# Optimization experiments

Hardware: AMD Instinct MI355X
Metric: run time of the kernel (lower is better)

Reference implementation:

```python
import jax, jax.numpy as jnp
import numpy as np

DIM = 1024
HIDDEN = 2816
NUM_EXPERTS = 8
TOP_K = 2
BATCH, SEQ = 2, 2048


def setup_inputs() -> dict:
    key = jax.random.key(0)
    kx, k1, k2, k3, kg = jax.random.split(key, 5)
    x = jax.random.normal(kx, (BATCH, SEQ, DIM), dtype=jnp.float32)
    # merged expert weights, layout (num_experts * hidden, dim) as in torch module
    w1 = jax.random.normal(k1, (NUM_EXPERTS * HIDDEN, DIM), dtype=jnp.float32) * 0.02
    w2 = jax.random.normal(k2, (NUM_EXPERTS * HIDDEN, DIM), dtype=jnp.float32) * 0.02
    w3 = jax.random.normal(k3, (NUM_EXPERTS * HIDDEN, DIM), dtype=jnp.float32) * 0.02
    gate_w = jax.random.normal(kg, (NUM_EXPERTS, DIM), dtype=jnp.float32) * 0.02
    return {"x": x, "w1": w1, "w2": w2, "w3": w3, "gate_w": gate_w}


def reference(x, w1, w2, w3, gate_w):
    input_shape = x.shape
    xt = x.reshape(-1, input_shape[-1])  # (T, D)
    T = xt.shape[0]
    # gating: softmax in fp32, top-k, renormalize selected weights
    logits = xt @ gate_w.T  # (T, E)
    probs = jax.nn.softmax(logits.astype(jnp.float32), axis=-1)
    weights, selected = jax.lax.top_k(probs, TOP_K)  # (T, K)
    weights = weights / jnp.sum(weights, axis=-1, keepdims=True)
    weights = weights.astype(x.dtype)
    # combine weights per expert: (T, E)
    combine = jnp.sum(jax.nn.one_hot(selected, NUM_EXPERTS, dtype=x.dtype) * weights[..., None], axis=1)
    # per-expert SwiGLU FFN: h = silu(x W1_e^T) * (x W3_e^T); out_e = h @ W2_e
    W1 = w1.reshape(NUM_EXPERTS, HIDDEN, DIM)
    W2 = w2.reshape(NUM_EXPERTS, HIDDEN, DIM)
    W3 = w3.reshape(NUM_EXPERTS, HIDDEN, DIM)
    y = jnp.zeros((T, DIM), dtype=x.dtype)
    for e in range(NUM_EXPERTS):  # fixed small expert loop
        h = jax.nn.silu(xt @ W1[e].T) * (xt @ W3[e].T)  # (T, H)
        y = y + (h @ W2[e]) * combine[:, e:e + 1]
    return y.reshape(input_shape)
```

## Files before the change

### kernel.cpp

```cpp
#include <hip/hip_runtime.h>
#include <cstddef>
#include <cstdint>

#define T_TOK 4096
#define DIM   1024
#define HID   2816
#define NE    8
#define TOPK  2
#define CAP   9216
#define NRT   72

#define BM 128
#define BN 64
#define BK 32

#define WS_COUNTS  0
#define WS_CURSORS 64
#define WS_OFFSETS 128
#define WS_TILE_E  256
#define WS_SEL     1024
#define WS_WTS     (WS_SEL  + T_TOK*2*4)
#define WS_ATOK    (WS_WTS  + T_TOK*2*4)
#define WS_AW      (WS_ATOK + CAP*4)
#define WS_H       140288

typedef __attribute__((ext_vector_type(8))) short bf16x8;
typedef __attribute__((ext_vector_type(4))) float f32x4;

__device__ __forceinline__ unsigned short f2bf(float f) {
  unsigned int u = __builtin_bit_cast(unsigned int, f);
  unsigned int r = u + 0x7FFFu + ((u >> 16) & 1u);
  return (unsigned short)(r >> 16);
}
__device__ __forceinline__ float bf2f(unsigned short s) {
  unsigned int u = ((unsigned int)s) << 16;
  return __builtin_bit_cast(float, u);
}
__device__ __forceinline__ void split2(float f, unsigned short& hi, unsigned short& lo) {
  hi = f2bf(f);
  lo = f2bf(f - bf2f(hi));
}

__device__ __forceinline__ int fragoff(int row, int k) {
  return ((row >> 4) << 9) + ((k >> 3) << 7) + ((row & 15) << 3) + (k & 7);
}

__global__ __launch_bounds__(256) void gate_kernel(
    const float* __restrict__ x, const float* __restrict__ gw,
    int* __restrict__ sel, float* __restrict__ wts, int* __restrict__ counts)
{
  const int wave = threadIdx.x >> 6;
  const int lane = threadIdx.x & 63;
  const int t = blockIdx.x * 4 + wave;

  const float* xr = x + (size_t)t * DIM;
  float acc[NE] = {0.f, 0.f, 0.f, 0.f, 0.f, 0.f, 0.f, 0.f};

#pragma unroll 4
  for (int j = 0; j < DIM / 64; ++j) {
    const int d = lane + 64 * j;
    const float xv = xr[d];
#pragma unroll
    for (int e = 0; e < NE; ++e) acc[e] = fmaf(xv, gw[e * DIM + d], acc[e]);
  }
#pragma unroll
  for (int m = 32; m > 0; m >>= 1) {
#pragma unroll
    for (int e = 0; e < NE; ++e) acc[e] += __shfl_xor(acc[e], m, 64);
  }

  if (lane == 0) {
    float mx = acc[0];
#pragma unroll
    for (int e = 1; e < NE; ++e) mx = fmaxf(mx, acc[e]);
    float ex[NE];
#pragma unroll
    for (int e = 0; e < NE; ++e) ex[e] = __expf(acc[e] - mx);
    int e0 = 0; float p0 = ex[0];
#pragma unroll
    for (int e = 1; e < NE; ++e) if (ex[e] > p0) { p0 = ex[e]; e0 = e; }
    int e1 = -1; float p1 = -1.f;
#pragma unroll
    for (int e = 0; e < NE; ++e) if (e != e0 && ex[e] > p1) { p1 = ex[e]; e1 = e; }
    const float inv = 1.f / (p0 + p1);
    sel[2 * t + 0] = e0; sel[2 * t + 1] = e1;
    wts[2 * t + 0] = p0 * inv; wts[2 * t + 1] = p1 * inv;
    atomicAdd(&counts[e0], 1);
    atomicAdd(&counts[e1], 1);
  }
}

__global__ void offsets_kernel(const int* __restrict__ counts,
                               int* __restrict__ offsets, int* __restrict__ cursors,
                               int* __restrict__ tile_e)
{
  if (threadIdx.x == 0 && blockIdx.x == 0) {
    int off = 0;
    for (int e = 0; e < NE; ++e) {
      offsets[e] = off;
      cursors[e] = off;
      off += (counts[e] + 127) & ~127;
    }
    offsets[NE] = off;
    for (int t = 0; t < NRT; ++t) {
      const int r = t * BM;
      int ee = 0;
      while (ee < NE - 1 && r >= offsets[ee + 1]) ++ee;
      tile_e[t] = ee;
    }
  }
}

__global__ __launch_bounds__(256) void scatter_kernel(
    const int* __restrict__ sel, const float* __restrict__ wts,
    int* __restrict__ cursors, int* __restrict__ atok, float* __restrict__ aw)
{
  const int t = blockIdx.x * 256 + threadIdx.x;
  if (t < T_TOK) {
#pragma unroll
    for (int k = 0; k < TOPK; ++k) {
      const int e = sel[2 * t + k];
      const int pos = atomicAdd(&cursors[e], 1);
      atok[pos] = t;
      aw[pos] = wts[2 * t + k];
    }
  }
}

__global__ __launch_bounds__(256, 2) void gemm1_kernel(
    const float* __restrict__ x, const float* __restrict__ w1,
    const float* __restrict__ w3, const int* __restrict__ atok,
    const int* __restrict__ tile_e, float* __restrict__ h,
    int hc0, int CH)
{
  __shared__ unsigned short sAh[4096], sAl[4096];
  __shared__ unsigned short sB1h[2048], sB1l[2048];
  __shared__ unsigned short sB3h[2048], sB3l[2048];
  __shared__ int sToks[BM];

  const int rt = blockIdx.x, ct = blockIdx.y;
  const int row0 = rt * BM;
  const int tid = threadIdx.x;
  const int lane = tid & 63;
  const int wv = tid >> 6, wr = wv >> 1, wc = wv & 1;
  const int e = tile_e[rt];

  if (tid < BM) {
    const int tk = atok[row0 + tid];
    sToks[tid] = tk < 0 ? 0 : tk;
  }
  __syncthreads();

  const int c4 = tid & 7;
  const int srow = tid >> 3;
  const float* ax[4];
  int aadr[4];
#pragma unroll
  for (int i = 0; i < 4; ++i) {
    const int r = srow + 32 * i;
    ax[i] = x + (size_t)sToks[r] * DIM + c4 * 4;
    aadr[i] = fragoff(r, c4 * 4);
  }
  const float* W1p = w1 + ((size_t)e * HID + hc0 + ct * BN) * DIM;
  const float* W3p = w3 + ((size_t)e * HID + hc0 + ct * BN) * DIM;
  const float* b1p[2]; const float* b3p[2];
  int badr[2];
#pragma unroll
  for (int i = 0; i < 2; ++i) {
    const int c = srow + 32 * i;
    b1p[i] = W1p + (size_t)c * DIM + c4 * 4;
    b3p[i] = W3p + (size_t)c * DIM + c4 * 4;
    badr[i] = fragoff(c, c4 * 4);
  }

  const f32x4 vz = {0.f, 0.f, 0.f, 0.f};
  f32x4 acc1[4][2], acc3[4][2];
#pragma unroll
  for (int i = 0; i < 4; ++i)
#pragma unroll
    for (int j = 0; j < 2; ++j) { acc1[i][j] = vz; acc3[i][j] = vz; }

  for (int kt = 0; kt < DIM / BK; ++kt) {
    const int k0 = kt * BK;
    float4 av[4], b1v[2], b3v[2];
#pragma unroll
    for (int i = 0; i < 4; ++i) av[i] = *(const float4*)(ax[i] + k0);
#pragma unroll
    for (int i = 0; i < 2; ++i) {
      b1v[i] = *(const float4*)(b1p[i] + k0);
      b3v[i] = *(const float4*)(b3p[i] + k0);
    }
    __syncthreads();
#pragma unroll
    for (int i = 0; i < 4; ++i) {
      ushort4 hi, lo;
      split2(av[i].x, hi.x, lo.x); split2(av[i].y, hi.y, lo.y);
      split2(av[i].z, hi.z, lo.z); split2(av[i].w, hi.w, lo.w);
      *(ushort4*)&sAh[aadr[i]] = hi;  *(ushort4*)&sAl[aadr[i]] = lo;
    }
#pragma unroll
    for (int i = 0; i < 2; ++i) {
      ushort4 hi, lo;
      split2(b1v[i].x, hi.x, lo.x); split2(b1v[i].y, hi.y, lo.y);
      split2(b1v[i].z, hi.z, lo.z); split2(b1v[i].w, hi.w, lo.w);
      *(ushort4*)&sB1h[badr[i]] = hi; *(ushort4*)&sB1l[badr[i]] = lo;
      split2(b3v[i].x, hi.x, lo.x); split2(b3v[i].y, hi.y, lo.y);
      split2(b3v[i].z, hi.z, lo.z); split2(b3v[i].w, hi.w, lo.w);
      *(ushort4*)&sB3h[badr[i]] = hi; *(ushort4*)&sB3l[badr[i]] = lo;
    }
    __syncthreads();

    bf16x8 ah[4], al[4], g1h[2], g1l[2], g3h[2], g3l[2];
#pragma unroll
    for (int ar = 0; ar < 4; ++ar) {
      const int rb = wr * 4 + ar;
      ah[ar] = *(const bf16x8*)&sAh[rb * 512 + lane * 8];
      al[ar] = *(const bf16x8*)&sAl[rb * 512 + lane * 8];
    }
#pragma unroll
    for (int bc = 0; bc < 2; ++bc) {
      const int cb = wc * 2 + bc;
      g1h[bc] = *(const bf16x8*)&sB1h[cb * 512 + lane * 8];
      g1l[bc] = *(const bf16x8*)&sB1l[cb * 512 + lane * 8];
      g3h[bc] = *(const bf16x8*)&sB3h[cb * 512 + lane * 8];
      g3l[bc] = *(const bf16x8*)&sB3l[cb * 512 + lane * 8];
    }
#pragma unroll
    for (int ar = 0; ar < 4; ++ar)
#pragma unroll
      for (int bc = 0; bc < 2; ++bc) {
        acc1[ar][bc] = __builtin_amdgcn_mfma_f32_16x16x32_bf16(ah[ar], g1h[bc], acc1[ar][bc], 0, 0, 0);
        acc1[ar][bc] = __builtin_amdgcn_mfma_f32_16x16x32_bf16(ah[ar], g1l[bc], acc1[ar][bc], 0, 0, 0);
        acc1[ar][bc] = __builtin_amdgcn_mfma_f32_16x16x32_bf16(al[ar], g1h[bc], acc1[ar][bc], 0, 0, 0);
        acc3[ar][bc] = __builtin_amdgcn_mfma_f32_16x16x32_bf16(ah[ar], g3h[bc], acc3[ar][bc], 0, 0, 0);
        acc3[ar][bc] = __builtin_amdgcn_mfma_f32_16x16x32_bf16(ah[ar], g3l[bc], acc3[ar][bc], 0, 0, 0);
        acc3[ar][bc] = __builtin_amdgcn_mfma_f32_16x16x32_bf16(al[ar], g3h[bc], acc3[ar][bc], 0, 0, 0);
      }
  }

#pragma unroll
  for (int ar = 0; ar < 4; ++ar)
#pragma unroll
    for (int bc = 0; bc < 2; ++bc)
#pragma unroll
      for (int r = 0; r < 4; ++r) {
        const int row = row0 + wr * 64 + ar * 16 + (lane >> 4) * 4 + r;
        const int col = ct * BN + wc * 32 + bc * 16 + (lane & 15);
        const float g = acc1[ar][bc][r];
        const float u = acc3[ar][bc][r];
        const float s = g / (1.f + __expf(-g));
        h[(size_t)row * CH + col] = s * u;
      }
}

__global__ __launch_bounds__(256, 2) void gemm2_kernel(
    const float* __restrict__ h, const float* __restrict__ w2,
    const int* __restrict__ atok, const float* __restrict__ aw,
    const int* __restrict__ tile_e, float* __restrict__ y,
    int hc0, int CH)
{
  __shared__ unsigned short sAh[4096], sAl[4096];
  __shared__ unsigned short sBh[2048], sBl[2048];

  const int rt = blockIdx.x, ct = blockIdx.y;
  const int row0 = rt * BM;
  const int tid = threadIdx.x;
  const int lane = tid & 63;
  const int wv = tid >> 6, wr = wv >> 1, wc = wv & 1;
  const int e = tile_e[rt];

  const int c4 = tid & 7;
  const int srow = tid >> 3;
  const float* ax[4];
  int aadr[4];
#pragma unroll
  for (int i = 0; i < 4; ++i) {
    const int r = srow + 32 * i;
    ax[i] = h + (size_t)(row0 + r) * CH + c4 * 4;
    aadr[i] = fragoff(r, c4 * 4);
  }
  const int n = tid & 63;
  const int kq0 = tid >> 6;
  const float* W2p = w2 + ((size_t)e * HID + hc0) * DIM + (size_t)ct * BN + n;

  const f32x4 vz = {0.f, 0.f, 0.f, 0.f};
  f32x4 acc[4][2];
#pragma unroll
  for (int i = 0; i < 4; ++i)
#pragma unroll
    for (int j = 0; j < 2; ++j) acc[i][j] = vz;

  for (int kt = 0; kt < CH / BK; ++kt) {
    const int k0 = kt * BK;
    float4 av[4];
    float bv[2][4];
#pragma unroll
    for (int i = 0; i < 4; ++i) av[i] = *(const float4*)(ax[i] + k0);
#pragma unroll
    for (int i = 0; i < 2; ++i) {
      const int kq = kq0 + 4 * i;
#pragma unroll
      for (int q = 0; q < 4; ++q)
        bv[i][q] = W2p[(size_t)(k0 + kq * 4 + q) * DIM];
    }
    __syncthreads();
#pragma unroll
    for (int i = 0; i < 4; ++i) {
      ushort4 hi, lo;
      split2(av[i].x, hi.x, lo.x); split2(av[i].y, hi.y, lo.y);
      split2(av[i].z, hi.z, lo.z); split2(av[i].w, hi.w, lo.w);
      *(ushort4*)&sAh[aadr[i]] = hi;  *(ushort4*)&sAl[aadr[i]] = lo;
    }
#pragma unroll
    for (int i = 0; i < 2; ++i) {
      const int kq = kq0 + 4 * i;
      const int ba = ((n >> 4) << 9) + ((kq >> 1) << 7) + ((n & 15) << 3) + ((kq & 1) << 2);
      ushort4 hi, lo;
      split2(bv[i][0], hi.x, lo.x); split2(bv[i][1], hi.y, lo.y);
      split2(bv[i][2], hi.z, lo.z); split2(bv[i][3], hi.w, lo.w);
      *(ushort4*)&sBh[ba] = hi; *(ushort4*)&sBl[ba] = lo;
    }
    __syncthreads();

    bf16x8 ah[4], al[4], bh_[2], bl_[2];
#pragma unroll
    for (int ar = 0; ar < 4; ++ar) {
      const int rb = wr * 4 + ar;
      ah[ar] = *(const bf16x8*)&sAh[rb * 512 + lane * 8];
      al[ar] = *(const bf16x8*)&sAl[rb * 512 + lane * 8];
    }
#pragma unroll
    for (int bc = 0; bc < 2; ++bc) {
      const int cb = wc * 2 + bc;
      bh_[bc] = *(const bf16x8*)&sBh[cb * 512 + lane * 8];
      bl_[bc] = *(const bf16x8*)&sBl[cb * 512 + lane * 8];
    }
#pragma unroll
    for (int ar = 0; ar < 4; ++ar)
#pragma unroll
      for (int bc = 0; bc < 2; ++bc) {
        acc[ar][bc] = __builtin_amdgcn_mfma_f32_16x16x32_bf16(ah[ar], bh_[bc], acc[ar][bc], 0, 0, 0);
        acc[ar][bc] = __builtin_amdgcn_mfma_f32_16x16x32_bf16(ah[ar], bl_[bc], acc[ar][bc], 0, 0, 0);
        acc[ar][bc] = __builtin_amdgcn_mfma_f32_16x16x32_bf16(al[ar], bh_[bc], acc[ar][bc], 0, 0, 0);
      }
  }

#pragma unroll
  for (int ar = 0; ar < 4; ++ar)
#pragma unroll
    for (int r = 0; r < 4; ++r) {
      const int grow = row0 + wr * 64 + ar * 16 + (lane >> 4) * 4 + r;
      const int tok = atok[grow];
      if (tok >= 0) {
        const float wgt = aw[grow];
#pragma unroll
        for (int bc = 0; bc < 2; ++bc) {
          const int col = ct * BN + wc * 32 + bc * 16 + (lane & 15);
          atomicAdd(y + (size_t)tok * DIM + col, acc[ar][bc][r] * wgt);
        }
      }
    }
}

extern "C" void kernel_launch(void* const* d_in, const int* in_sizes, int n_in,
                              void* d_out, int out_size, void* d_ws, size_t ws_size,
                              hipStream_t stream) {
  const float* x  = (const float*)d_in[0];
  const float* w1 = (const float*)d_in[1];
  const float* w2 = (const float*)d_in[2];
  const float* w3 = (const float*)d_in[3];
  const float* gw = (const float*)d_in[4];
  float* y = (float*)d_out;

  char* ws = (char*)d_ws;
  int*   counts  = (int*)(ws + WS_COUNTS);
  int*   cursors = (int*)(ws + WS_CURSORS);
  int*   offsets = (int*)(ws + WS_OFFSETS);
  int*   tile_e  = (int*)(ws + WS_TILE_E);
  int*   sel     = (int*)(ws + WS_SEL);
  float* wts     = (float*)(ws + WS_WTS);
  int*   atok    = (int*)(ws + WS_ATOK);
  float* aw      = (float*)(ws + WS_AW);
  float* h       = (float*)(ws + WS_H);

  static const int chs[6] = {2816, 1408, 704, 256, 128, 64};
  int CH = 64;
  for (int i = 0; i < 6; ++i) {
    if ((size_t)WS_H + (size_t)CAP * (size_t)chs[i] * 4ull <= ws_size) { CH = chs[i]; break; }
  }

  hipMemsetAsync(counts, 0, 8 * sizeof(int), stream);
  hipMemsetAsync(atok, 0xFF, CAP * sizeof(int), stream);
  hipMemsetAsync(y, 0, (size_t)T_TOK * DIM * sizeof(float), stream);

  gate_kernel<<<T_TOK / 4, 256, 0, stream>>>(x, gw, sel, wts, counts);
  offsets_kernel<<<1, 64, 0, stream>>>(counts, offsets, cursors, tile_e);
  scatter_kernel<<<T_TOK / 256, 256, 0, stream>>>(sel, wts, cursors, atok, aw);

  for (int hc0 = 0; hc0 < HID; hc0 += CH) {
    gemm1_kernel<<<dim3(NRT, CH / BN), 256, 0, stream>>>(x, w1, w3, atok, tile_e, h, hc0, CH);
    gemm2_kernel<<<dim3(NRT, DIM / BN), 256, 0, stream>>>(h, w2, atok, aw, tile_e, y, hc0, CH);
  }
}
```

Baseline: 1.114 ms.

## Pre-split inputs and weights to bf16 hi/lo images, load via global_load_lds

```diff
diff --git a/kernel.cpp b/kernel.cpp
--- a/kernel.cpp
+++ b/kernel.cpp
@@ -9,23 +9,29 @@
 #define TOPK  2
 #define CAP   9216
 #define NRT   72
-
-#define BM 128
-#define BN 64
-#define BK 32
+#define BM    128
+#define BN    64
+#define BK    32
 
 #define WS_COUNTS  0
 #define WS_CURSORS 64
 #define WS_OFFSETS 128
 #define WS_TILE_E  256
 #define WS_SEL     1024
-#define WS_WTS     (WS_SEL  + T_TOK*2*4)
-#define WS_ATOK    (WS_WTS  + T_TOK*2*4)
-#define WS_AW      (WS_ATOK + CAP*4)
-#define WS_H       140288
+#define WS_WTS     33792
+#define WS_ATOK    66560
+#define WS_AW      103424
+#define WS_XHI     140288
+#define WS_XLO     8528896
+#define WS_IMG     16917504
 
 typedef __attribute__((ext_vector_type(8))) short bf16x8;
+typedef __attribute__((ext_vector_type(8))) unsigned short u16x8;
 typedef __attribute__((ext_vector_type(4))) float f32x4;
+
+#define GL16(gp, lp) __builtin_amdgcn_global_load_lds( \
+    (const __attribute__((address_space(1))) unsigned int*)(gp), \
+    (__attribute__((address_space(3))) unsigned int*)(lp), 16, 0, 0)
 
 __device__ __forceinline__ unsigned short f2bf(float f) {
   unsigned int u = __builtin_bit_cast(unsigned int, f);
@@ -41,10 +47,6 @@
   lo = f2bf(f - bf2f(hi));
 }
 
-__device__ __forceinline__ int fragoff(int row, int k) {
-  return ((row >> 4) << 9) + ((k >> 3) << 7) + ((row & 15) << 3) + (k & 7);
-}
-
 __global__ __launch_bounds__(256) void gate_kernel(
     const float* __restrict__ x, const float* __restrict__ gw,
     int* __restrict__ sel, float* __restrict__ wts, int* __restrict__ counts)
@@ -52,10 +54,8 @@
   const int wave = threadIdx.x >> 6;
   const int lane = threadIdx.x & 63;
   const int t = blockIdx.x * 4 + wave;
-
   const float* xr = x + (size_t)t * DIM;
   float acc[NE] = {0.f, 0.f, 0.f, 0.f, 0.f, 0.f, 0.f, 0.f};
-
 #pragma unroll 4
   for (int j = 0; j < DIM / 64; ++j) {
     const int d = lane + 64 * j;
@@ -68,7 +68,6 @@
 #pragma unroll
     for (int e = 0; e < NE; ++e) acc[e] += __shfl_xor(acc[e], m, 64);
   }
-
   if (lane == 0) {
     float mx = acc[0];
 #pragma unroll
@@ -127,51 +126,108 @@
   }
 }
 
-__global__ __launch_bounds__(256, 2) void gemm1_kernel(
-    const float* __restrict__ x, const float* __restrict__ w1,
-    const float* __restrict__ w3, const int* __restrict__ atok,
-    const int* __restrict__ tile_e, float* __restrict__ h,
-    int hc0, int CH)
-{
-  __shared__ unsigned short sAh[4096], sAl[4096];
-  __shared__ unsigned short sB1h[2048], sB1l[2048];
-  __shared__ unsigned short sB3h[2048], sB3l[2048];
+__global__ __launch_bounds__(256) void convert_x_kernel(
+    const float* __restrict__ x, unsigned short* __restrict__ xhi,
+    unsigned short* __restrict__ xlo)
+{
+  const size_t t = (size_t)blockIdx.x * 256 + threadIdx.x;
+  const float* s = x + t * 8;
+  u16x8 hi, lo;
+#pragma unroll
+  for (int q = 0; q < 8; ++q) {
+    unsigned short h, l;
+    split2(s[q], h, l);
+    hi[q] = h; lo[q] = l;
+  }
+  *(u16x8*)&xhi[t * 8] = hi;
+  *(u16x8*)&xlo[t * 8] = lo;
+}
+
+__global__ __launch_bounds__(256) void convert_w13_kernel(
+    const float* __restrict__ w, unsigned short* __restrict__ img,
+    int hc0, int nct1)
+{
+  const int f = blockIdx.x * 256 + threadIdx.x;
+  const int ks = f & 3;
+  int t = f >> 2;
+  const int n15 = t & 15; t >>= 4;
+  const int nb = t & 3;   t >>= 2;
+  const int kt = t & 31;  t >>= 5;
+  const int ct = t % nct1;
+  const int e  = t / nct1;
+  const float* src = w + ((size_t)e * HID + hc0 + ct * 64 + nb * 16 + n15) * DIM + kt * 32 + ks * 8;
+  u16x8 hi, lo;
+#pragma unroll
+  for (int q = 0; q < 8; ++q) {
+    unsigned short h, l;
+    split2(src[q], h, l);
+    hi[q] = h; lo[q] = l;
+  }
+  const size_t tile = ((size_t)(e * nct1 + ct) * 32 + kt) * 4096;
+  const int off = nb * 512 + ks * 128 + n15 * 8;
+  *(u16x8*)&img[tile + off] = hi;
+  *(u16x8*)&img[tile + 2048 + off] = lo;
+}
+
+__global__ __launch_bounds__(256) void convert_w2_kernel(
+    const float* __restrict__ w2, unsigned short* __restrict__ img,
+    int hc0, int nkt2)
+{
+  const int f = blockIdx.x * 256 + threadIdx.x;
+  const int n15 = f & 15;
+  int t = f >> 4;
+  const int ks = t & 3; t >>= 2;
+  const int nb = t & 3; t >>= 2;
+  const int kt = t % nkt2; t /= nkt2;
+  const int ct2 = t & 15;
+  const int e = t >> 4;
+  const float* src = w2 + ((size_t)e * HID + hc0 + kt * 32 + ks * 8) * DIM + ct2 * 64 + nb * 16 + n15;
+  u16x8 hi, lo;
+#pragma unroll
+  for (int q = 0; q < 8; ++q) {
+    unsigned short h, l;
+    split2(src[(size_t)q * DIM], h, l);
+    hi[q] = h; lo[q] = l;
+  }
+  const size_t tile = ((size_t)(e * 16 + ct2) * nkt2 + kt) * 4096;
+  const int off = nb * 512 + ks * 128 + n15 * 8;
+  *(u16x8*)&img[tile + off] = hi;
+  *(u16x8*)&img[tile + 2048 + off] = lo;
+}
+
+__global__ __launch_bounds__(256) void gemm1_kernel(
+    const unsigned short* __restrict__ xhi, const unsigned short* __restrict__ xlo,
+    const unsigned short* __restrict__ w1img, const unsigned short* __restrict__ w3img,
+    const int* __restrict__ atok, const int* __restrict__ tile_e,
+    unsigned short* __restrict__ himg, int nct1)
+{
+  __shared__ __align__(16) unsigned short sAh[4096], sAl[4096];
+  __shared__ __align__(16) unsigned short sB1h[2048], sB1l[2048], sB3h[2048], sB3l[2048];
   __shared__ int sToks[BM];
 
-  const int rt = blockIdx.x, ct = blockIdx.y;
-  const int row0 = rt * BM;
-  const int tid = threadIdx.x;
-  const int lane = tid & 63;
+  const int orig = blockIdx.x;
+  const int wg = (orig & 7) * (gridDim.x >> 3) + (orig >> 3);
+  const int ct = wg / NRT, rt = wg % NRT;
+  const int nkt2 = nct1 * 2;
+  const int tid = threadIdx.x, lane = tid & 63;
   const int wv = tid >> 6, wr = wv >> 1, wc = wv & 1;
   const int e = tile_e[rt];
 
   if (tid < BM) {
-    const int tk = atok[row0 + tid];
+    const int tk = atok[rt * BM + tid];
     sToks[tid] = tk < 0 ? 0 : tk;
   }
   __syncthreads();
 
-  const int c4 = tid & 7;
-  const int srow = tid >> 3;
-  const float* ax[4];
-  int aadr[4];
-#pragma unroll
-  for (int i = 0; i < 4; ++i) {
-    const int r = srow + 32 * i;
-    ax[i] = x + (size_t)sToks[r] * DIM + c4 * 4;
-    aadr[i] = fragoff(r, c4 * 4);
-  }
-  const float* W1p = w1 + ((size_t)e * HID + hc0 + ct * BN) * DIM;
-  const float* W3p = w3 + ((size_t)e * HID + hc0 + ct * BN) * DIM;
-  const float* b1p[2]; const float* b3p[2];
-  int badr[2];
+  const int rb0 = wv * 2;
+  size_t asrc[2];
 #pragma unroll
   for (int i = 0; i < 2; ++i) {
-    const int c = srow + 32 * i;
-    b1p[i] = W1p + (size_t)c * DIM + c4 * 4;
-    b3p[i] = W3p + (size_t)c * DIM + c4 * 4;
-    badr[i] = fragoff(c, c4 * 4);
-  }
+    const int row = (rb0 + i) * 16 + (lane & 15);
+    asrc[i] = (size_t)sToks[row] * DIM + ((lane >> 4) * 8);
+  }
+  const size_t btile0 = ((size_t)(e * nct1 + ct) * 32) * 4096;
+  const size_t boff = btile0 + wv * 512 + (size_t)lane * 8;
 
   const f32x4 vz = {0.f, 0.f, 0.f, 0.f};
   f32x4 acc1[4][2], acc3[4][2];
@@ -181,33 +237,17 @@
     for (int j = 0; j < 2; ++j) { acc1[i][j] = vz; acc3[i][j] = vz; }
 
   for (int kt = 0; kt < DIM / BK; ++kt) {
-    const int k0 = kt * BK;
-    float4 av[4], b1v[2], b3v[2];
-#pragma unroll
-    for (int i = 0; i < 4; ++i) av[i] = *(const float4*)(ax[i] + k0);
+    __syncthreads();
 #pragma unroll
     for (int i = 0; i < 2; ++i) {
-      b1v[i] = *(const float4*)(b1p[i] + k0);
-      b3v[i] = *(const float4*)(b3p[i] + k0);
-    }
-    __syncthreads();
-#pragma unroll
-    for (int i = 0; i < 4; ++i) {
-      ushort4 hi, lo;
-      split2(av[i].x, hi.x, lo.x); split2(av[i].y, hi.y, lo.y);
-      split2(av[i].z, hi.z, lo.z); split2(av[i].w, hi.w, lo.w);
-      *(ushort4*)&sAh[aadr[i]] = hi;  *(ushort4*)&sAl[aadr[i]] = lo;
-    }
-#pragma unroll
-    for (int i = 0; i < 2; ++i) {
-      ushort4 hi, lo;
-      split2(b1v[i].x, hi.x, lo.x); split2(b1v[i].y, hi.y, lo.y);
-      split2(b1v[i].z, hi.z, lo.z); split2(b1v[i].w, hi.w, lo.w);
-      *(ushort4*)&sB1h[badr[i]] = hi; *(ushort4*)&sB1l[badr[i]] = lo;
-      split2(b3v[i].x, hi.x, lo.x); split2(b3v[i].y, hi.y, lo.y);
-      split2(b3v[i].z, hi.z, lo.z); split2(b3v[i].w, hi.w, lo.w);
-      *(ushort4*)&sB3h[badr[i]] = hi; *(ushort4*)&sB3l[badr[i]] = lo;
-    }
+      GL16(xhi + asrc[i] + kt * 32, &sAh[(rb0 + i) * 512]);
+      GL16(xlo + asrc[i] + kt * 32, &sAl[(rb0 + i) * 512]);
+    }
+    const size_t bk = boff + (size_t)kt * 4096;
+    GL16(w1img + bk,        &sB1h[wv * 512]);
+    GL16(w1img + bk + 2048, &sB1l[wv * 512]);
+    GL16(w3img + bk,        &sB3h[wv * 512]);
+    GL16(w3img + bk + 2048, &sB3l[wv * 512]);
     __syncthreads();
 
     bf16x8 ah[4], al[4], g1h[2], g1l[2], g3h[2], g3l[2];
@@ -238,50 +278,44 @@
       }
   }
 
+  const size_t hbase = ((size_t)rt * nkt2 + (ct * 2 + wc)) * 8192;
 #pragma unroll
   for (int ar = 0; ar < 4; ++ar)
 #pragma unroll
     for (int bc = 0; bc < 2; ++bc)
 #pragma unroll
       for (int r = 0; r < 4; ++r) {
-        const int row = row0 + wr * 64 + ar * 16 + (lane >> 4) * 4 + r;
-        const int col = ct * BN + wc * 32 + bc * 16 + (lane & 15);
         const float g = acc1[ar][bc][r];
         const float u = acc3[ar][bc][r];
         const float s = g / (1.f + __expf(-g));
-        h[(size_t)row * CH + col] = s * u;
+        unsigned short h_, l_;
+        split2(s * u, h_, l_);
+        const int idx = (wr * 4 + ar) * 512 + (bc * 2 + ((lane >> 3) & 1)) * 128
+                      + ((lane >> 4) * 4 + r) * 8 + (lane & 7);
+        himg[hbase + idx] = h_;
+        himg[hbase + 4096 + idx] = l_;
       }
 }
 
-__global__ __launch_bounds__(256, 2) void gemm2_kernel(
-    const float* __restrict__ h, const float* __restrict__ w2,
+__global__ __launch_bounds__(256) void gemm2_kernel(
+    const unsigned short* __restrict__ himg, const unsigned short* __restrict__ w2img,
     const int* __restrict__ atok, const float* __restrict__ aw,
-    const int* __restrict__ tile_e, float* __restrict__ y,
-    int hc0, int CH)
-{
-  __shared__ unsigned short sAh[4096], sAl[4096];
-  __shared__ unsigned short sBh[2048], sBl[2048];
-
-  const int rt = blockIdx.x, ct = blockIdx.y;
-  const int row0 = rt * BM;
-  const int tid = threadIdx.x;
-  const int lane = tid & 63;
+    const int* __restrict__ tile_e, float* __restrict__ y, int nkt2)
+{
+  __shared__ __align__(16) unsigned short sAh[4096], sAl[4096];
+  __shared__ __align__(16) unsigned short sBh[2048], sBl[2048];
+
+  const int orig = blockIdx.x;
+  const int wg = (orig & 7) * (gridDim.x >> 3) + (orig >> 3);
+  const int ct2 = wg / NRT, rt = wg % NRT;
+  const int tid = threadIdx.x, lane = tid & 63;
   const int wv = tid >> 6, wr = wv >> 1, wc = wv & 1;
   const int e = tile_e[rt];
 
-  const int c4 = tid & 7;
-  const int srow = tid >> 3;
-  const float* ax[4];
-  int aadr[4];
-#pragma unroll
-  for (int i = 0; i < 4; ++i) {
-    const int r = srow + 32 * i;
-    ax[i] = h + (size_t)(row0 + r) * CH + c4 * 4;
-    aadr[i] = fragoff(r, c4 * 4);
-  }
-  const int n = tid & 63;
-  const int kq0 = tid >> 6;
-  const float* W2p = w2 + ((size_t)e * HID + hc0) * DIM + (size_t)ct * BN + n;
+  const int rb0 = wv * 2;
+  const size_t atile0 = (size_t)rt * nkt2 * 8192;
+  const size_t btile0 = ((size_t)(e * 16 + ct2) * nkt2) * 4096;
+  const size_t lane8 = (size_t)lane * 8;
 
   const f32x4 vz = {0.f, 0.f, 0.f, 0.f};
   f32x4 acc[4][2];
@@ -290,36 +324,17 @@
 #pragma unroll
     for (int j = 0; j < 2; ++j) acc[i][j] = vz;
 
-  for (int kt = 0; kt < CH / BK; ++kt) {
-    const int k0 = kt * BK;
-    float4 av[4];
-    float bv[2][4];
-#pragma unroll
-    for (int i = 0; i < 4; ++i) av[i] = *(const float4*)(ax[i] + k0);
+  for (int kt = 0; kt < nkt2; ++kt) {
+    __syncthreads();
+    const size_t ab = atile0 + (size_t)kt * 8192;
 #pragma unroll
     for (int i = 0; i < 2; ++i) {
-      const int kq = kq0 + 4 * i;
-#pragma unroll
-      for (int q = 0; q < 4; ++q)
-        bv[i][q] = W2p[(size_t)(k0 + kq * 4 + q) * DIM];
-    }
-    __syncthreads();
-#pragma unroll
-    for (int i = 0; i < 4; ++i) {
-      ushort4 hi, lo;
-      split2(av[i].x, hi.x, lo.x); split2(av[i].y, hi.y, lo.y);
-      split2(av[i].z, hi.z, lo.z); split2(av[i].w, hi.w, lo.w);
-      *(ushort4*)&sAh[aadr[i]] = hi;  *(ushort4*)&sAl[aadr[i]] = lo;
-    }
-#pragma unroll
-    for (int i = 0; i < 2; ++i) {
-      const int kq = kq0 + 4 * i;
-      const int ba = ((n >> 4) << 9) + ((kq >> 1) << 7) + ((n & 15) << 3) + ((kq & 1) << 2);
-      ushort4 hi, lo;
-      split2(bv[i][0], hi.x, lo.x); split2(bv[i][1], hi.y, lo.y);
-      split2(bv[i][2], hi.z, lo.z); split2(bv[i][3], hi.w, lo.w);
-      *(ushort4*)&sBh[ba] = hi; *(ushort4*)&sBl[ba] = lo;
-    }
+      GL16(himg + ab + (rb0 + i) * 512 + lane8,        &sAh[(rb0 + i) * 512]);
+      GL16(himg + ab + 4096 + (rb0 + i) * 512 + lane8, &sAl[(rb0 + i) * 512]);
+    }
+    const size_t bb = btile0 + (size_t)kt * 4096 + wv * 512 + lane8;
+    GL16(w2img + bb,        &sBh[wv * 512]);
+    GL16(w2img + bb + 2048, &sBl[wv * 512]);
     __syncthreads();
 
     bf16x8 ah[4], al[4], bh_[2], bl_[2];
@@ -349,13 +364,13 @@
   for (int ar = 0; ar < 4; ++ar)
 #pragma unroll
     for (int r = 0; r < 4; ++r) {
-      const int grow = row0 + wr * 64 + ar * 16 + (lane >> 4) * 4 + r;
+      const int grow = rt * BM + wr * 64 + ar * 16 + (lane >> 4) * 4 + r;
       const int tok = atok[grow];
       if (tok >= 0) {
         const float wgt = aw[grow];
 #pragma unroll
         for (int bc = 0; bc < 2; ++bc) {
-          const int col = ct * BN + wc * 32 + bc * 16 + (lane & 15);
+          const int col = ct2 * BN + wc * 32 + bc * 16 + (lane & 15);
           atomicAdd(y + (size_t)tok * DIM + col, acc[ar][bc][r] * wgt);
         }
       }
@@ -381,13 +396,21 @@
   float* wts     = (float*)(ws + WS_WTS);
   int*   atok    = (int*)(ws + WS_ATOK);
   float* aw      = (float*)(ws + WS_AW);
-  float* h       = (float*)(ws + WS_H);
+  unsigned short* xhi = (unsigned short*)(ws + WS_XHI);
+  unsigned short* xlo = (unsigned short*)(ws + WS_XLO);
 
   static const int chs[6] = {2816, 1408, 704, 256, 128, 64};
   int CH = 64;
   for (int i = 0; i < 6; ++i) {
-    if ((size_t)WS_H + (size_t)CAP * (size_t)chs[i] * 4ull <= ws_size) { CH = chs[i]; break; }
-  }
+    const size_t need = (size_t)WS_IMG + (size_t)chs[i] * 135168ull;
+    if (need <= ws_size) { CH = chs[i]; break; }
+  }
+  const int nct1 = CH / 64, nkt2 = CH / 32;
+  const size_t wimg_b = (size_t)CH * 32768ull;
+  unsigned short* w1img = (unsigned short*)(ws + WS_IMG);
+  unsigned short* w3img = (unsigned short*)(ws + WS_IMG + wimg_b);
+  unsigned short* w2img = (unsigned short*)(ws + WS_IMG + 2 * wimg_b);
+  unsigned short* himg  = (unsigned short*)(ws + WS_IMG + 3 * wimg_b);
 
   hipMemsetAsync(counts, 0, 8 * sizeof(int), stream);
   hipMemsetAsync(atok, 0xFF, CAP * sizeof(int), stream);
@@ -396,9 +419,14 @@
   gate_kernel<<<T_TOK / 4, 256, 0, stream>>>(x, gw, sel, wts, counts);
   offsets_kernel<<<1, 64, 0, stream>>>(counts, offsets, cursors, tile_e);
   scatter_kernel<<<T_TOK / 256, 256, 0, stream>>>(sel, wts, cursors, atok, aw);
+  convert_x_kernel<<<(T_TOK * DIM / 8) / 256, 256, 0, stream>>>(x, xhi, xlo);
 
   for (int hc0 = 0; hc0 < HID; hc0 += CH) {
-    gemm1_kernel<<<dim3(NRT, CH / BN), 256, 0, stream>>>(x, w1, w3, atok, tile_e, h, hc0, CH);
-    gemm2_kernel<<<dim3(NRT, DIM / BN), 256, 0, stream>>>(h, w2, atok, aw, tile_e, y, hc0, CH);
-  }
-}
+    const int wblk = 8 * nct1 * 32;
+    convert_w13_kernel<<<wblk, 256, 0, stream>>>(w1, w1img, hc0, nct1);
+    convert_w13_kernel<<<wblk, 256, 0, stream>>>(w3, w3img, hc0, nct1);
+    convert_w2_kernel<<<128 * nkt2, 256, 0, stream>>>(w2, w2img, hc0, nkt2);
+    gemm1_kernel<<<NRT * nct1, 256, 0, stream>>>(xhi, xlo, w1img, w3img, atok, tile_e, himg, nct1);
+    gemm2_kernel<<<NRT * 16, 256, 0, stream>>>(himg, w2img, atok, aw, tile_e, y, nkt2);
+  }
+}
```

After: 1.179 ms. 1.06x slower.
